# Performance work log

Hardware: AMD Instinct MI355X
Metric: run time of the kernel (lower is better)

Reference implementation:

```python
import jax, jax.numpy as jnp
import numpy as np

D_MODEL = 1024
MAX_LEN = 2048
ORDER = 2
BATCH = 4
SEQ = 2048


def setup_inputs() -> dict:
    key = jax.random.key(0)
    k1, k2, k3, k4 = jax.random.split(key, 4)
    x = jax.random.normal(k1, (BATCH, SEQ, D_MODEL), dtype=jnp.float32)
    # torch Linear(d, d*(order+1)): weight [out,in]; we store transposed [in,out]
    proj_w = jax.random.normal(k2, (D_MODEL, D_MODEL * (ORDER + 1)), dtype=jnp.float32) * (D_MODEL ** -0.5)
    proj_b = jax.random.normal(k3, (D_MODEL * (ORDER + 1),), dtype=jnp.float32) * 0.02
    filter_time = jax.random.normal(k4, (ORDER, 1, MAX_LEN, D_MODEL), dtype=jnp.float32) / (MAX_LEN ** 0.5)
    return {"x": x, "proj_w": proj_w, "proj_b": proj_b, "filter_time": filter_time}


def reference(x, proj_w, proj_b, filter_time):
    B, L, D = x.shape
    order, _, max_length, _ = filter_time.shape
    fft_size = 2 * max_length
    # projection -> [B, L, order+1, D]
    p = (jnp.einsum('bld,de->ble', x, proj_w) + proj_b).reshape(B, L, order + 1, D)
    v = p[:, :, 0, :]  # value stream [B, L, D]
    for stage in range(order):
        # zero-padding to fft_size is implicit via n=fft_size; real FFT is the
        # real-valued-optimized equivalent of fft->complex-mul->ifft.real
        vf = jnp.fft.rfft(v, n=fft_size, axis=1)                      # [B, fft/2+1, D]
        ff = jnp.fft.rfft(filter_time[stage], n=fft_size, axis=1)    # [1, fft/2+1, D]
        conv = jnp.fft.irfft(vf * ff, n=fft_size, axis=1)[:, :L, :]  # causal slice
        v = conv * p[:, :, stage + 1, :]                              # gate
    return v
```

## Files before the change

kernel.cpp:

```cpp
#include <hip/hip_runtime.h>
#include <hip/hip_bf16.h>

#define B_     4
#define L_     2048
#define D_     1024
#define MAXLEN 2048
#define N_     3072
#define K_     1024
#define KP     40

typedef __attribute__((ext_vector_type(8))) short short8;
typedef __attribute__((ext_vector_type(4))) short short4v;
typedef __attribute__((ext_vector_type(4))) float f32x4;

__device__ __forceinline__ short f2bf(float x) {
    return __builtin_bit_cast(short, (__bf16)x);
}
__device__ __forceinline__ float bf2f(short h) {
    return (float)__builtin_bit_cast(__bf16, h);
}

__global__ __launch_bounds__(256) void wsplit_kernel(
    const float* __restrict__ W, short* __restrict__ WtH, short* __restrict__ WtL)
{
    __shared__ float lds[64][65];
    const int n0 = blockIdx.x * 64;
    const int k0 = blockIdx.y * 64;
    const int t  = threadIdx.x;
    const int nc = t & 63;
#pragma unroll
    for (int i = 0; i < 16; ++i) {
        const int kr = i * 4 + (t >> 6);
        lds[kr][nc] = W[(size_t)(k0 + kr) * N_ + n0 + nc];
    }
    __syncthreads();
    const int kg = (t & 15) * 4;
#pragma unroll
    for (int r = 0; r < 4; ++r) {
        const int nr = (t >> 4) + r * 16;
        short4v hv, lv;
#pragma unroll
        for (int j = 0; j < 4; ++j) {
            const float x = lds[kg + j][nr];
            const short h = f2bf(x);
            hv[j] = h;
            lv[j] = f2bf(x - bf2f(h));
        }
        const size_t o = (size_t)(n0 + nr) * K_ + k0 + kg;
        *(short4v*)&WtH[o] = hv;
        *(short4v*)&WtL[o] = lv;
    }
}

__global__ __launch_bounds__(256) void gemm_mfma_kernel(
    const float* __restrict__ X, const short* __restrict__ WtH,
    const short* __restrict__ WtL, const float* __restrict__ bias,
    float* __restrict__ p0, float* __restrict__ p1, float* __restrict__ p2)
{
    __shared__ __align__(16) short Ah[128][KP];
    __shared__ __align__(16) short Al[128][KP];
    __shared__ __align__(16) short Bh[128][KP];
    __shared__ __align__(16) short Bl[128][KP];

    const int tid = threadIdx.x;
    const int m0 = blockIdx.y * 128;
    const int n0 = blockIdx.x * 128;

    const int lane = tid & 63;
    const int wave = tid >> 6;
    const int wr = wave >> 1;
    const int wc = wave & 1;
    const int fr = lane & 15;
    const int fq = lane >> 4;

    const int srow  = tid >> 1;
    const int shalf = (tid & 1) * 16;

    f32x4 acc[4][4];
#pragma unroll
    for (int m = 0; m < 4; ++m)
#pragma unroll
        for (int n = 0; n < 4; ++n) acc[m][n] = (f32x4){0.f, 0.f, 0.f, 0.f};

    const float* xp  = &X[(size_t)(m0 + srow) * K_ + shalf];
    const short* bhp = &WtH[(size_t)(n0 + srow) * K_ + shalf];
    const short* blp = &WtL[(size_t)(n0 + srow) * K_ + shalf];

    for (int k0 = 0; k0 < K_; k0 += 32) {
        float xv[16];
        *(float4*)&xv[0]  = *(const float4*)&xp[k0];
        *(float4*)&xv[4]  = *(const float4*)&xp[k0 + 4];
        *(float4*)&xv[8]  = *(const float4*)&xp[k0 + 8];
        *(float4*)&xv[12] = *(const float4*)&xp[k0 + 12];
        short8 ah[2], al[2];
#pragma unroll
        for (int g = 0; g < 2; ++g)
#pragma unroll
            for (int j = 0; j < 8; ++j) {
                const float x = xv[g * 8 + j];
                const short h = f2bf(x);
                ah[g][j] = h;
                al[g][j] = f2bf(x - bf2f(h));
            }
        *(short8*)&Ah[srow][shalf]     = ah[0];
        *(short8*)&Ah[srow][shalf + 8] = ah[1];
        *(short8*)&Al[srow][shalf]     = al[0];
        *(short8*)&Al[srow][shalf + 8] = al[1];
        *(short8*)&Bh[srow][shalf]     = *(const short8*)&bhp[k0];
        *(short8*)&Bh[srow][shalf + 8] = *(const short8*)&bhp[k0 + 8];
        *(short8*)&Bl[srow][shalf]     = *(const short8*)&blp[k0];
        *(short8*)&Bl[srow][shalf + 8] = *(const short8*)&blp[k0 + 8];
        __syncthreads();

        short8 aH[4], aL[4], bH[4], bL[4];
#pragma unroll
        for (int m = 0; m < 4; ++m) {
            aH[m] = *(const short8*)&Ah[wr * 64 + m * 16 + fr][fq * 8];
            aL[m] = *(const short8*)&Al[wr * 64 + m * 16 + fr][fq * 8];
        }
#pragma unroll
        for (int n = 0; n < 4; ++n) {
            bH[n] = *(const short8*)&Bh[wc * 64 + n * 16 + fr][fq * 8];
            bL[n] = *(const short8*)&Bl[wc * 64 + n * 16 + fr][fq * 8];
        }
#pragma unroll
        for (int m = 0; m < 4; ++m)
#pragma unroll
            for (int n = 0; n < 4; ++n) {
                acc[m][n] = __builtin_amdgcn_mfma_f32_16x16x32_bf16(aH[m], bH[n], acc[m][n], 0, 0, 0);
                acc[m][n] = __builtin_amdgcn_mfma_f32_16x16x32_bf16(aH[m], bL[n], acc[m][n], 0, 0, 0);
                acc[m][n] = __builtin_amdgcn_mfma_f32_16x16x32_bf16(aL[m], bH[n], acc[m][n], 0, 0, 0);
            }
        __syncthreads();
    }

    const int s = n0 >> 10;
    float* outp = (s == 0) ? p0 : ((s == 1) ? p1 : p2);
    const int csub = n0 & 1023;
#pragma unroll
    for (int n = 0; n < 4; ++n) {
        const int gcol = wc * 64 + n * 16 + fr;
        const float bv = bias[n0 + gcol];
        const int col = csub + gcol;
#pragma unroll
        for (int m = 0; m < 4; ++m) {
            const int rowb = m0 + wr * 64 + m * 16 + fq * 4;
#pragma unroll
            for (int j = 0; j < 4; ++j)
                outp[(size_t)(rowb + j) * D_ + col] = acc[m][n][j] + bv;
        }
    }
}

__global__ __launch_bounds__(256, 2) void conv_stage_kernel(
    const float* __restrict__ vin, const float* __restrict__ filt,
    const float* __restrict__ gate, float* __restrict__ vout)
{
    __shared__ float v_lds[64][64];
    __shared__ float f4[48][64][4];

    const int d0 = blockIdx.x * 64;
    const int yp = blockIdx.y;
    const int b  = blockIdx.z;
    const int tid = threadIdx.x;
    const int dl = tid & 63;
    const int rg = tid >> 6;
    const int r0 = rg * 32;

    const int sr = tid >> 4;
    const int sc = (tid & 15) * 4;
    const int fch = tid & 63;
    const int fq0 = tid >> 6;

    const float* vin_b = vin + (size_t)b * L_ * D_;

#define FWQ(i) fwq[((i) >> 2) % 12][(i) & 3]

    for (int half = 0; half < 2; ++half) {
        const int yt = (half == 0) ? yp : (15 - yp);
        const int l0 = yt * 128;
        const int ntiles = 2 * yt + 2;
        int c_cur = l0 % 192;

        __syncthreads();
        {
#pragma unroll
            for (int s = 0; s < 4; ++s) {
                const float4 q = *(const float4*)&vin_b[(size_t)(sr + 16*s) * D_ + d0 + sc];
                *(float4*)&v_lds[sr + 16*s][sc] = q;
            }
            const int base0 = l0 - 63;
#pragma unroll
            for (int s = 0; s < 12; ++s) {
                const int qr = fq0 + 4*s;
                int qsg = (c_cur >> 2) + qr; if (qsg >= 48) qsg -= 48;
                f32x4 q;
#pragma unroll
                for (int e = 0; e < 4; ++e) {
                    const int a = base0 + 4*qr + e;
                    float fv = 0.f;
                    if (a >= 0 && a < MAXLEN) fv = filt[(size_t)a * D_ + d0 + fch];
                    q[e] = fv;
                }
                *(f32x4*)&f4[qsg][fch][0] = q;
            }
        }
        __syncthreads();

        float acc[32];
#pragma unroll
        for (int j = 0; j < 32; ++j) acc[j] = 0.f;

        for (int ti = 0; ti < ntiles; ++ti) {
            int base4 = (c_cur + r0) >> 2;
            if (base4 >= 48) base4 -= 48;

            f32x4 fwq[12];
#pragma unroll
            for (int q = 15; q <= 23; ++q) {
                int x4 = base4 + q; if (x4 >= 48) x4 -= 48;
                fwq[q % 12] = *(const f32x4*)&f4[x4][dl][0];
            }
            float vv[2][4];
#pragma unroll
            for (int u = 0; u < 4; ++u) vv[0][u] = v_lds[u][dl];

#pragma unroll
            for (int si = 0; si < 16; ++si) {
                const int tb = 4 * si;
                if (si < 15) {
                    const int q = 14 - si;
                    int x4 = base4 + q; if (x4 >= 48) x4 -= 48;
                    fwq[q % 12] = *(const f32x4*)&f4[x4][dl][0];
#pragma unroll
                    for (int u = 0; u < 4; ++u)
                        vv[(si + 1) & 1][u] = v_lds[tb + 4 + u][dl];
                }
#pragma unroll
                for (int u = 0; u < 4; ++u)
#pragma unroll
                    for (int j = 0; j < 32; ++j)
                        acc[j] += vv[si & 1][u] * FWQ(63 - tb + j - u);
            }

            if (ti + 1 < ntiles) {
                int c_next = c_cur - 64; if (c_next < 0) c_next += 192;
                const int t0n = 64 * (ti + 1);
                const int basen = l0 - t0n - 63;
                __syncthreads();
                float4 tv[4];
                f32x4 tf[4];
#pragma unroll
                for (int s = 0; s < 4; ++s)
                    tv[s] = *(const float4*)&vin_b[(size_t)(t0n + sr + 16*s) * D_ + d0 + sc];
#pragma unroll
                for (int s = 0; s < 4; ++s) {
                    const int qr = fq0 + 4*s;
#pragma unroll
                    for (int e = 0; e < 4; ++e) {
                        const int a = basen + 4*qr + e;
                        float fv = 0.f;
                        if (a >= 0 && a < MAXLEN) fv = filt[(size_t)a * D_ + d0 + fch];
                        tf[s][e] = fv;
                    }
                }
#pragma unroll
                for (int s = 0; s < 4; ++s)
                    *(float4*)&v_lds[sr + 16*s][sc] = tv[s];
#pragma unroll
                for (int s = 0; s < 4; ++s) {
                    const int qsg = (c_next >> 2) + fq0 + 4*s;
                    *(f32x4*)&f4[qsg][fch][0] = tf[s];
                }
                __syncthreads();
                c_cur = c_next;
            }
        }

        const size_t off = (size_t)b * L_ * D_ + (size_t)l0 * D_ + d0 + dl;
#pragma unroll
        for (int j = 0; j < 32; ++j) {
            const size_t idx = off + (size_t)(r0 + j) * D_;
            vout[idx] = acc[j] * gate[idx];
        }
    }
#undef FWQ
}

extern "C" void kernel_launch(void* const* d_in, const int* in_sizes, int n_in,
                              void* d_out, int out_size, void* d_ws, size_t ws_size,
                              hipStream_t stream) {
    const float* x  = (const float*)d_in[0];
    const float* w  = (const float*)d_in[1];
    const float* bb = (const float*)d_in[2];
    const float* ft = (const float*)d_in[3];
    float* out = (float*)d_out;

    float* p0 = (float*)d_ws;
    float* p1 = p0 + (size_t)B_ * L_ * D_;
    float* p2 = p1 + (size_t)B_ * L_ * D_;

    short* WtH = (short*)d_out;
    short* WtL = WtH + (size_t)N_ * K_;

    wsplit_kernel<<<dim3(N_ / 64, K_ / 64), 256, 0, stream>>>(w, WtH, WtL);

    gemm_mfma_kernel<<<dim3(N_ / 128, (B_ * L_) / 128), 256, 0, stream>>>(
        x, WtH, WtL, bb, p0, p1, p2);

    conv_stage_kernel<<<dim3(D_ / 64, 8, B_), 256, 0, stream>>>(
        p0, ft, p1, p1);

    conv_stage_kernel<<<dim3(D_ / 64, 8, B_), 256, 0, stream>>>(
        p1, ft + (size_t)MAXLEN * D_, p2, out);
}
```

Baseline: 688.9 us.

## Double the conv block to 512 threads and prefetch the next tile into registers

The causal-convolution kernel now runs 512 threads per block, so each thread accumulates 16 output rows instead of 32, which shrinks the accumulator and filter-window register arrays. The global loads for the next time tile (values and filter taps) are issued into registers one tile ahead, so their latency overlaps the current tile's FMA loop instead of sitting between two barriers. Interior tiles skip the filter bounds check. The cost is that each filter value read from LDS now serves fewer FMAs, and the larger block synchronises more threads at each barrier.

```diff
diff --git a/kernel.cpp b/kernel.cpp
--- a/kernel.cpp
+++ b/kernel.cpp
@@ -152,7 +152,7 @@
     }
 }
 
-__global__ __launch_bounds__(256, 2) void conv_stage_kernel(
+__global__ __launch_bounds__(512, 4) void conv_stage_kernel(
     const float* __restrict__ vin, const float* __restrict__ filt,
     const float* __restrict__ gate, float* __restrict__ vout)
 {
@@ -165,16 +165,16 @@
     const int tid = threadIdx.x;
     const int dl = tid & 63;
     const int rg = tid >> 6;
-    const int r0 = rg * 32;
-
-    const int sr = tid >> 4;
-    const int sc = (tid & 15) * 4;
+    const int r0 = rg * 16;
+
+    const int vr = tid >> 4;
+    const int vc = (tid & 15) * 4;
     const int fch = tid & 63;
     const int fq0 = tid >> 6;
 
     const float* vin_b = vin + (size_t)b * L_ * D_;
 
-#define FWQ(i) fwq[((i) >> 2) % 12][(i) & 3]
+#define FWQ(i) fwq[((i) >> 2) & 7][(i) & 3]
 
     for (int half = 0; half < 2; ++half) {
         const int yt = (half == 0) ? yp : (15 - yp);
@@ -185,21 +185,22 @@
         __syncthreads();
         {
 #pragma unroll
-            for (int s = 0; s < 4; ++s) {
-                const float4 q = *(const float4*)&vin_b[(size_t)(sr + 16*s) * D_ + d0 + sc];
-                *(float4*)&v_lds[sr + 16*s][sc] = q;
+            for (int s = 0; s < 2; ++s) {
+                const float4 q = *(const float4*)&vin_b[(size_t)(vr + 32*s) * D_ + d0 + vc];
+                *(float4*)&v_lds[vr + 32*s][vc] = q;
             }
             const int base0 = l0 - 63;
 #pragma unroll
-            for (int s = 0; s < 12; ++s) {
-                const int qr = fq0 + 4*s;
+            for (int s = 0; s < 6; ++s) {
+                const int qr = fq0 + 8*s;
                 int qsg = (c_cur >> 2) + qr; if (qsg >= 48) qsg -= 48;
                 f32x4 q;
 #pragma unroll
                 for (int e = 0; e < 4; ++e) {
                     const int a = base0 + 4*qr + e;
                     float fv = 0.f;
-                    if (a >= 0 && a < MAXLEN) fv = filt[(size_t)a * D_ + d0 + fch];
+                    if (a >= 0 && a < MAXLEN)
+                        fv = filt[(size_t)a * D_ + d0 + fch];
                     q[e] = fv;
                 }
                 *(f32x4*)&f4[qsg][fch][0] = q;
@@ -207,19 +208,39 @@
         }
         __syncthreads();
 
-        float acc[32];
-#pragma unroll
-        for (int j = 0; j < 32; ++j) acc[j] = 0.f;
+        float4 pv[2];
+        f32x4 pf[2];
+        {
+#pragma unroll
+            for (int s = 0; s < 2; ++s)
+                pv[s] = *(const float4*)&vin_b[(size_t)(64 + vr + 32*s) * D_ + d0 + vc];
+            const int base1 = l0 - 127;
+#pragma unroll
+            for (int s = 0; s < 2; ++s) {
+                const int qr = fq0 + 8*s;
+#pragma unroll
+                for (int e = 0; e < 4; ++e) {
+                    const int a = base1 + 4*qr + e;
+                    float fv = 0.f;
+                    if (a >= 0) fv = filt[(size_t)a * D_ + d0 + fch];
+                    pf[s][e] = fv;
+                }
+            }
+        }
+
+        float acc[16];
+#pragma unroll
+        for (int j = 0; j < 16; ++j) acc[j] = 0.f;
 
         for (int ti = 0; ti < ntiles; ++ti) {
             int base4 = (c_cur + r0) >> 2;
             if (base4 >= 48) base4 -= 48;
 
-            f32x4 fwq[12];
-#pragma unroll
-            for (int q = 15; q <= 23; ++q) {
+            f32x4 fwq[8];
+#pragma unroll
+            for (int q = 15; q <= 19; ++q) {
                 int x4 = base4 + q; if (x4 >= 48) x4 -= 48;
-                fwq[q % 12] = *(const f32x4*)&f4[x4][dl][0];
+                fwq[q & 7] = *(const f32x4*)&f4[x4][dl][0];
             }
             float vv[2][4];
 #pragma unroll
@@ -231,7 +252,7 @@
                 if (si < 15) {
                     const int q = 14 - si;
                     int x4 = base4 + q; if (x4 >= 48) x4 -= 48;
-                    fwq[q % 12] = *(const f32x4*)&f4[x4][dl][0];
+                    fwq[q & 7] = *(const f32x4*)&f4[x4][dl][0];
 #pragma unroll
                     for (int u = 0; u < 4; ++u)
                         vv[(si + 1) & 1][u] = v_lds[tb + 4 + u][dl];
@@ -239,47 +260,57 @@
 #pragma unroll
                 for (int u = 0; u < 4; ++u)
 #pragma unroll
-                    for (int j = 0; j < 32; ++j)
+                    for (int j = 0; j < 16; ++j)
                         acc[j] += vv[si & 1][u] * FWQ(63 - tb + j - u);
             }
 
             if (ti + 1 < ntiles) {
                 int c_next = c_cur - 64; if (c_next < 0) c_next += 192;
-                const int t0n = 64 * (ti + 1);
-                const int basen = l0 - t0n - 63;
                 __syncthreads();
-                float4 tv[4];
-                f32x4 tf[4];
-#pragma unroll
-                for (int s = 0; s < 4; ++s)
-                    tv[s] = *(const float4*)&vin_b[(size_t)(t0n + sr + 16*s) * D_ + d0 + sc];
-#pragma unroll
-                for (int s = 0; s < 4; ++s) {
-                    const int qr = fq0 + 4*s;
-#pragma unroll
-                    for (int e = 0; e < 4; ++e) {
-                        const int a = basen + 4*qr + e;
-                        float fv = 0.f;
-                        if (a >= 0 && a < MAXLEN) fv = filt[(size_t)a * D_ + d0 + fch];
-                        tf[s][e] = fv;
+#pragma unroll
+                for (int s = 0; s < 2; ++s)
+                    *(float4*)&v_lds[vr + 32*s][vc] = pv[s];
+#pragma unroll
+                for (int s = 0; s < 2; ++s) {
+                    const int qsg = (c_next >> 2) + fq0 + 8*s;
+                    *(f32x4*)&f4[qsg][fch][0] = pf[s];
+                }
+                __syncthreads();
+                if (ti + 2 < ntiles) {
+                    const int t0n = 64 * (ti + 2);
+#pragma unroll
+                    for (int s = 0; s < 2; ++s)
+                        pv[s] = *(const float4*)&vin_b[(size_t)(t0n + vr + 32*s) * D_ + d0 + vc];
+                    const int basen = l0 - t0n - 63;
+                    if (basen >= 0) {
+#pragma unroll
+                        for (int s = 0; s < 2; ++s) {
+                            const int qr = fq0 + 8*s;
+#pragma unroll
+                            for (int e = 0; e < 4; ++e)
+                                pf[s][e] = filt[(size_t)(basen + 4*qr + e) * D_ + d0 + fch];
+                        }
+                    } else {
+#pragma unroll
+                        for (int s = 0; s < 2; ++s) {
+                            const int qr = fq0 + 8*s;
+#pragma unroll
+                            for (int e = 0; e < 4; ++e) {
+                                const int a = basen + 4*qr + e;
+                                float fv = 0.f;
+                                if (a >= 0) fv = filt[(size_t)a * D_ + d0 + fch];
+                                pf[s][e] = fv;
+                            }
+                        }
                     }
                 }
-#pragma unroll
-                for (int s = 0; s < 4; ++s)
-                    *(float4*)&v_lds[sr + 16*s][sc] = tv[s];
-#pragma unroll
-                for (int s = 0; s < 4; ++s) {
-                    const int qsg = (c_next >> 2) + fq0 + 4*s;
-                    *(f32x4*)&f4[qsg][fch][0] = tf[s];
-                }
-                __syncthreads();
                 c_cur = c_next;
             }
         }
 
         const size_t off = (size_t)b * L_ * D_ + (size_t)l0 * D_ + d0 + dl;
 #pragma unroll
-        for (int j = 0; j < 32; ++j) {
+        for (int j = 0; j < 16; ++j) {
             const size_t idx = off + (size_t)(r0 + j) * D_;
             vout[idx] = acc[j] * gate[idx];
         }
@@ -308,9 +339,9 @@
     gemm_mfma_kernel<<<dim3(N_ / 128, (B_ * L_) / 128), 256, 0, stream>>>(
         x, WtH, WtL, bb, p0, p1, p2);
 
-    conv_stage_kernel<<<dim3(D_ / 64, 8, B_), 256, 0, stream>>>(
+    conv_stage_kernel<<<dim3(D_ / 64, 8, B_), 512, 0, stream>>>(
         p0, ft, p1, p1);
 
-    conv_stage_kernel<<<dim3(D_ / 64, 8, B_), 256, 0, stream>>>(
+    conv_stage_kernel<<<dim3(D_ / 64, 8, B_), 512, 0, stream>>>(
         p1, ft + (size_t)MAXLEN * D_, p2, out);
 }
```

New measurement: 1.965 ms. +185.2%, slower.
